# Kernel tuning notes

Hardware: AMD Instinct MI355X
Metric: run time of the kernel (lower is better)

## Reference

```python
import jax, jax.numpy as jnp
import numpy as np
from functools import partial

B, L, D = 4, 1024, 512
H = 8                 # attention heads
DIN = 2 * D           # mamba d_inner (expand=2)
N = 16                # mamba d_state
K = 4                 # mamba d_conv
R = 32                # dt_rank = ceil(D/16)


def setup_inputs() -> dict:
    key = jax.random.key(0)
    ks = jax.random.split(key, 24)
    s = 0.02
    nrm = lambda k, sh: (jax.random.normal(k, sh, dtype=jnp.float32) * s)
    inp = {
        'x':       jax.random.normal(ks[0], (B, L, D), dtype=jnp.float32),
        # attention projections
        'Wq': nrm(ks[1], (D, D)), 'bq': jnp.zeros((D,), jnp.float32),
        'Wk': nrm(ks[2], (D, D)), 'bk': jnp.zeros((D,), jnp.float32),
        'Wv': nrm(ks[3], (D, D)), 'bv': jnp.zeros((D,), jnp.float32),
        'Wo': nrm(ks[4], (D, D)), 'bo': jnp.zeros((D,), jnp.float32),
        # layernorms
        'ln1_g': jnp.ones((D,), jnp.float32), 'ln1_b': jnp.zeros((D,), jnp.float32),
        'ln2_g': jnp.ones((D,), jnp.float32), 'ln2_b': jnp.zeros((D,), jnp.float32),
        # mamba params
        'm_Win':   nrm(ks[5], (D, 2 * DIN)),            # in_proj (no bias)
        'm_conv_w': nrm(ks[6], (DIN, 1, K)),            # depthwise causal conv
        'm_conv_b': jnp.zeros((DIN,), jnp.float32),
        'm_Wx':    nrm(ks[7], (DIN, R + 2 * N)),        # x_proj (no bias)
        'm_Wdt':   nrm(ks[8], (R, DIN)),                # dt_proj
        'm_bdt':   jnp.full((DIN,), 0.5, jnp.float32),
        'm_Alog':  jnp.log(jnp.broadcast_to(jnp.arange(1, N + 1, dtype=jnp.float32), (DIN, N))).copy(),
        'm_D':     jnp.ones((DIN,), jnp.float32),
        'm_Wout':  nrm(ks[9], (DIN, D)),                # out_proj (no bias)
    }
    return inp


def _layernorm(x, g, b, eps=1e-5):
    mu = jnp.mean(x, axis=-1, keepdims=True)
    var = jnp.var(x, axis=-1, keepdims=True)
    return (x - mu) * jax.lax.rsqrt(var + eps) * g + b


def _mamba(x, Win, conv_w, conv_b, Wx, Wdt, bdt, Alog, Dp, Wout):
    b, l, _ = x.shape
    xz = x @ Win                           # [B,L,2*DIN]
    xi, z = xz[..., :DIN], xz[..., DIN:]
    # causal depthwise conv over time
    xt = jnp.transpose(xi, (0, 2, 1))      # [B,DIN,L]
    xt = jax.lax.conv_general_dilated(
        xt, conv_w, window_strides=(1,), padding=[(K - 1, 0)],
        feature_group_count=DIN, dimension_numbers=('NCH', 'OIH', 'NCH'))
    xc = jax.nn.silu(jnp.transpose(xt, (0, 2, 1)) + conv_b)   # [B,L,DIN]
    # input-dependent SSM params
    dbl = xc @ Wx                          # [B,L,R+2N]
    dt = jax.nn.softplus(dbl[..., :R] @ Wdt + bdt)            # [B,L,DIN]
    Bm = dbl[..., R:R + N]                 # [B,L,N]
    Cm = dbl[..., R + N:]                  # [B,L,N]
    A = -jnp.exp(Alog)                     # [DIN,N]
    dA = jnp.exp(dt[..., None] * A)                     # [B,L,DIN,N]
    dBx = (dt * xc)[..., None] * Bm[:, :, None, :]      # [B,L,DIN,N]

    def step(h, t):
        dA_t, dBx_t, C_t = t
        h = h * dA_t + dBx_t               # [B,DIN,N]
        y = jnp.einsum('bdn,bn->bd', h, C_t)
        return h, y

    h0 = jnp.zeros((b, DIN, N), xc.dtype)
    _, ys = jax.lax.scan(step, h0, (jnp.swapaxes(dA, 0, 1),
                                    jnp.swapaxes(dBx, 0, 1),
                                    jnp.swapaxes(Cm, 0, 1)))
    y = jnp.swapaxes(ys, 0, 1)             # [B,L,DIN]
    y = y + xc * Dp
    y = y * jax.nn.silu(z)
    return y @ Wout                        # [B,L,D]


def reference(x, Wq, bq, Wk, bk, Wv, bv, Wo, bo, ln1_g, ln1_b, ln2_g, ln2_b,
              m_Win, m_conv_w, m_conv_b, m_Wx, m_Wdt, m_bdt, m_Alog, m_D, m_Wout):
    b, l, d = x.shape
    E = d // H
    q = (x @ Wq + bq).reshape(b, l, H, E)
    k = (x @ Wk + bk).reshape(b, l, H, E)
    v = (x @ Wv + bv).reshape(b, l, H, E)
    scores = jnp.einsum('blhe,bshe->bhls', q, k) * (E ** -0.5)
    attn = jax.nn.softmax(scores, axis=-1)                    # [B,H,L,L]
    o = jnp.einsum('bhls,bshe->blhe', attn, v).reshape(b, l, d)
    new_x = o @ Wo + bo
    x1 = _layernorm(x + new_x, ln1_g, ln1_b)
    y = _mamba(x1, m_Win, m_conv_w, m_conv_b, m_Wx, m_Wdt, m_bdt, m_Alog, m_D, m_Wout)
    out = _layernorm(x1 + y, ln2_g, ln2_b)
    return out, attn
```

## Files before the change

kernel.cpp:

```cpp
#include <hip/hip_runtime.h>
#include <hip/hip_bf16.h>

#define BB 4
#define LL 1024
#define DD 512
#define HH 8
#define EE 64
#define DIN 1024
#define NN 16
#define KK 4
#define RR 32
#define BL (BB*LL)
#define CC 32
#define LC (LL/CC)
#define BDN (BB*DIN*NN)

using bf16 = __hip_bfloat16;
typedef __attribute__((ext_vector_type(8))) short short8;
typedef __attribute__((ext_vector_type(4))) float f32x4;

__device__ __forceinline__ float ldf(const float* p) { return *p; }
__device__ __forceinline__ float ldf(const bf16* p) { return __bfloat162float(*p); }
__device__ __forceinline__ void stf(float* p, float v) { *p = v; }
__device__ __forceinline__ void stf(bf16* p, float v) { *p = __float2bfloat16(v); }
__device__ __forceinline__ short f2bs(float f) { bf16 h = __float2bfloat16(f); return *(short*)&h; }

__global__ void cvt_k(const float* __restrict__ in, bf16* __restrict__ out, int n)
{
    int i = blockIdx.x * 256 + threadIdx.x;
    if (i < n) out[i] = __float2bfloat16(in[i]);
}

__global__ void tpw_k(const float* __restrict__ in, bf16* __restrict__ outT,
                      int Kd, int Nd)
{
    __shared__ float t[32][33];
    const int n0 = blockIdx.x * 32, k0 = blockIdx.y * 32;
    const int tx = threadIdx.x & 31, ty = threadIdx.x >> 5;
#pragma unroll
    for (int i = 0; i < 4; ++i)
        t[ty + 8 * i][tx] = in[(size_t)(k0 + ty + 8 * i) * Nd + n0 + tx];
    __syncthreads();
#pragma unroll
    for (int i = 0; i < 4; ++i)
        outT[(size_t)(n0 + ty + 8 * i) * Kd + k0 + tx] = __float2bfloat16(t[tx][ty + 8 * i]);
}

__global__ void tpv_k(const bf16* __restrict__ v, bf16* __restrict__ vT)
{
    __shared__ float t[32][33];
    const int l0 = blockIdx.x * 32;
    const int e0 = blockIdx.y * 32;
    const int bh = blockIdx.z, b = bh >> 3, h = bh & 7;
    const int tx = threadIdx.x & 31, ty = threadIdx.x >> 5;
#pragma unroll
    for (int i = 0; i < 4; ++i)
        t[ty + 8 * i][tx] = ldf(&v[(size_t)(b * LL + l0 + ty + 8 * i) * DD + h * EE + e0 + tx]);
    __syncthreads();
#pragma unroll
    for (int i = 0; i < 4; ++i)
        stf(&vT[(size_t)(bh * EE + e0 + ty + 8 * i) * LL + l0 + tx], t[tx][ty + 8 * i]);
}

template <typename TC>
__global__ void mfma_gemm_k(const bf16* __restrict__ A, int lda,
                            const bf16* __restrict__ Bt, int ldb,
                            const float* __restrict__ bias,
                            TC* __restrict__ C, int ldc, int Kd)
{
    const int lane = threadIdx.x & 63;
    const int w = threadIdx.x >> 6;
    const int m = lane & 15, quad = lane >> 4;
    const int m0 = blockIdx.y * 64 + (w >> 1) * 32;
    const int n0 = blockIdx.x * 64 + (w & 1) * 32;
    f32x4 acc[2][2] = {};
    const bf16* a0p = A + (size_t)(m0 + m) * lda + quad * 8;
    const bf16* a1p = a0p + (size_t)16 * lda;
    const bf16* b0p = Bt + (size_t)(n0 + m) * ldb + quad * 8;
    const bf16* b1p = b0p + (size_t)16 * ldb;
    for (int k = 0; k < Kd; k += 32) {
        short8 a0 = *(const short8*)(a0p + k);
        short8 a1 = *(const short8*)(a1p + k);
        short8 b0 = *(const short8*)(b0p + k);
        short8 b1 = *(const short8*)(b1p + k);
        acc[0][0] = __builtin_amdgcn_mfma_f32_16x16x32_bf16(a0, b0, acc[0][0], 0, 0, 0);
        acc[0][1] = __builtin_amdgcn_mfma_f32_16x16x32_bf16(a0, b1, acc[0][1], 0, 0, 0);
        acc[1][0] = __builtin_amdgcn_mfma_f32_16x16x32_bf16(a1, b0, acc[1][0], 0, 0, 0);
        acc[1][1] = __builtin_amdgcn_mfma_f32_16x16x32_bf16(a1, b1, acc[1][1], 0, 0, 0);
    }
#pragma unroll
    for (int i = 0; i < 2; ++i)
#pragma unroll
        for (int j = 0; j < 2; ++j)
#pragma unroll
            for (int r = 0; r < 4; ++r) {
                int row = m0 + i * 16 + quad * 4 + r;
                int col = n0 + j * 16 + (lane & 15);
                float vv = acc[i][j][r] + (bias ? bias[col] : 0.f);
                stf(&C[(size_t)row * ldc + col], vv);
            }
}

__global__ void attn_fused_k(const bf16* __restrict__ q, const bf16* __restrict__ k,
                             const bf16* __restrict__ vT,
                             float* __restrict__ attn, bf16* __restrict__ o)
{
    const int rt = blockIdx.x;
    const int bh = blockIdx.y, b = bh >> 3, h = bh & 7;
    const int w = threadIdx.x >> 6;
    const int lane = threadIdx.x & 63;
    const int m = lane & 15, quad = lane >> 4;
    __shared__ float pm[4][16], ps[4][16];
    __shared__ bf16 P[16][1032];

    const bf16* qp = q + (size_t)(b * LL + rt * 16 + m) * DD + h * EE + quad * 8;
    short8 a0 = *(const short8*)(qp);
    short8 a1 = *(const short8*)(qp + 32);

    f32x4 acc[16];
#pragma unroll
    for (int t = 0; t < 16; ++t) {
        int srow = w * 256 + t * 16 + m;
        const bf16* kp = k + (size_t)(b * LL + srow) * DD + h * EE + quad * 8;
        short8 b0 = *(const short8*)(kp);
        short8 b1 = *(const short8*)(kp + 32);
        f32x4 c = {};
        c = __builtin_amdgcn_mfma_f32_16x16x32_bf16(a0, b0, c, 0, 0, 0);
        c = __builtin_amdgcn_mfma_f32_16x16x32_bf16(a1, b1, c, 0, 0, 0);
        acc[t] = c;
    }

#pragma unroll
    for (int r = 0; r < 4; ++r) {
        float mx = -1e30f;
#pragma unroll
        for (int t = 0; t < 16; ++t) { acc[t][r] *= 0.125f; mx = fmaxf(mx, acc[t][r]); }
        mx = fmaxf(mx, __shfl_xor(mx, 1)); mx = fmaxf(mx, __shfl_xor(mx, 2));
        mx = fmaxf(mx, __shfl_xor(mx, 4)); mx = fmaxf(mx, __shfl_xor(mx, 8));
        if (m == 0) pm[w][quad * 4 + r] = mx;
    }
    __syncthreads();
#pragma unroll
    for (int r = 0; r < 4; ++r) {
        float mx = fmaxf(fmaxf(pm[0][quad * 4 + r], pm[1][quad * 4 + r]),
                         fmaxf(pm[2][quad * 4 + r], pm[3][quad * 4 + r]));
        float s = 0.f;
#pragma unroll
        for (int t = 0; t < 16; ++t) { float e = __expf(acc[t][r] - mx); acc[t][r] = e; s += e; }
        s += __shfl_xor(s, 1); s += __shfl_xor(s, 2);
        s += __shfl_xor(s, 4); s += __shfl_xor(s, 8);
        if (m == 0) ps[w][quad * 4 + r] = s;
    }
    __syncthreads();
#pragma unroll
    for (int r = 0; r < 4; ++r) {
        float tot = ps[0][quad * 4 + r] + ps[1][quad * 4 + r] + ps[2][quad * 4 + r] + ps[3][quad * 4 + r];
        float inv = 1.f / tot;
        int row = rt * 16 + quad * 4 + r;
        float* op = attn + ((size_t)bh * LL + row) * LL + w * 256 + (lane & 15);
#pragma unroll
        for (int t = 0; t < 16; ++t) {
            float pv = acc[t][r] * inv;
            op[t * 16] = pv;
            P[quad * 4 + r][w * 256 + t * 16 + m] = __float2bfloat16(pv);
        }
    }
    __syncthreads();

    const bf16* vp = vT + (size_t)(bh * EE + w * 16 + m) * LL + quad * 8;
    f32x4 oacc = {};
    for (int k0 = 0; k0 < LL; k0 += 32) {
        short8 af = *(const short8*)(&P[m][k0 + quad * 8]);
        short8 bf = *(const short8*)(vp + k0);
        oacc = __builtin_amdgcn_mfma_f32_16x16x32_bf16(af, bf, oacc, 0, 0, 0);
    }
#pragma unroll
    for (int r = 0; r < 4; ++r) {
        int row = rt * 16 + quad * 4 + r;
        stf(&o[(size_t)(b * LL + row) * DD + h * EE + w * 16 + (lane & 15)], oacc[r]);
    }
}

template <typename TA, typename TC, bool SP>
__global__ void gemm_k(const TA* __restrict__ A, int lda,
                       const float* __restrict__ B, int ldb,
                       const float* __restrict__ bias,
                       TC* __restrict__ C, int ldc,
                       int M, int N, int Kd)
{
    __shared__ float As[32][33];
    __shared__ float Bs[32][33];
    const int tid = threadIdx.x;
    const int tx = tid & 31;
    const int ty = tid >> 5;
    const int rowBase = blockIdx.y * 32;
    const int colBase = blockIdx.x * 32;
    float acc[4] = {0.f, 0.f, 0.f, 0.f};

    for (int k0 = 0; k0 < Kd; k0 += 32) {
#pragma unroll
        for (int i = 0; i < 4; ++i) {
            int r = ty + 8 * i;
            As[r][tx] = ldf(&A[(size_t)(rowBase + r) * lda + k0 + tx]);
            Bs[r][tx] = B[(size_t)(k0 + r) * ldb + colBase + tx];
        }
        __syncthreads();
#pragma unroll 8
        for (int kk = 0; kk < 32; ++kk) {
            float bv = Bs[kk][tx];
#pragma unroll
            for (int i = 0; i < 4; ++i) acc[i] += As[ty + 8 * i][kk] * bv;
        }
        __syncthreads();
    }
#pragma unroll
    for (int i = 0; i < 4; ++i) {
        int row = rowBase + ty + 8 * i;
        int col = colBase + tx;
        float r = acc[i] + (bias ? bias[col] : 0.f);
        if (SP) r = (r > 20.f) ? r : log1pf(__expf(r));
        stf(&C[(size_t)row * ldc + col], r);
    }
}

template <typename TA, typename TR, typename TO>
__global__ void add_ln_k(const TA* __restrict__ a, const TR* __restrict__ r,
                         const float* __restrict__ g, const float* __restrict__ be,
                         TO* __restrict__ out)
{
    const int row = blockIdx.x;
    const int tid = threadIdx.x;
    __shared__ float red[256];
    const size_t base = (size_t)row * DD;
    float v0 = ldf(&a[base + tid]) + ldf(&r[base + tid]);
    float v1 = ldf(&a[base + 256 + tid]) + ldf(&r[base + 256 + tid]);
    red[tid] = v0 + v1;
    __syncthreads();
    for (int off = 128; off > 0; off >>= 1) {
        if (tid < off) red[tid] += red[tid + off];
        __syncthreads();
    }
    const float mu = red[0] * (1.f / 512.f);
    __syncthreads();
    float d0 = v0 - mu, d1 = v1 - mu;
    red[tid] = d0 * d0 + d1 * d1;
    __syncthreads();
    for (int off = 128; off > 0; off >>= 1) {
        if (tid < off) red[tid] += red[tid + off];
        __syncthreads();
    }
    const float rs = rsqrtf(red[0] * (1.f / 512.f) + 1e-5f);
    stf(&out[base + tid], d0 * rs * g[tid] + be[tid]);
    stf(&out[base + 256 + tid], d1 * rs * g[tid + 256] + be[tid + 256]);
}

__global__ void conv_silu_k(const bf16* __restrict__ xz,
                            const float* __restrict__ w,
                            const float* __restrict__ cb,
                            bf16* __restrict__ xc)
{
    const int idx = blockIdx.x * 256 + threadIdx.x;
    const int c = idx & (DIN - 1);
    const int t = (idx >> 10) & (LL - 1);
    const int b = idx >> 20;
    float acc = cb[c];
    const bf16* xi = xz + (size_t)b * LL * (2 * DIN) + c;
#pragma unroll
    for (int j = 0; j < KK; ++j) {
        int tt = t - (KK - 1) + j;
        if (tt >= 0) acc += w[c * KK + j] * ldf(&xi[(size_t)tt * (2 * DIN)]);
    }
    stf(&xc[idx], acc / (1.f + __expf(-acc)));
}

__global__ void scan_p1_k(const bf16* __restrict__ dt, const bf16* __restrict__ xc,
                          const float* __restrict__ dbl, const float* __restrict__ Alog,
                          float* __restrict__ P, float* __restrict__ S)
{
    const int d = (blockIdx.x & 3) * 256 + threadIdx.x;
    const int c = blockIdx.x >> 2;
    const int b = blockIdx.y;
    float A[NN];
#pragma unroll
    for (int n = 0; n < NN; ++n) A[n] = -__expf(Alog[d * NN + n]);
    const int t0 = c * LC;
    const bf16* dt_b = dt + ((size_t)b * LL + t0) * DIN + d;
    const bf16* xc_b = xc + ((size_t)b * LL + t0) * DIN + d;
    const float* dbl_b = dbl + ((size_t)b * LL + t0) * 64 + RR;
    float h[NN];
#pragma unroll
    for (int n = 0; n < NN; ++n) h[n] = 0.f;
    float sdt = 0.f;
#pragma unroll 4
    for (int t = 0; t < LC; ++t) {
        float dtv = ldf(&dt_b[(size_t)t * DIN]);
        float xcv = ldf(&xc_b[(size_t)t * DIN]);
        float dtx = dtv * xcv;
        sdt += dtv;
#pragma unroll
        for (int n = 0; n < NN; ++n) {
            float dA = __expf(dtv * A[n]);
            h[n] = h[n] * dA + dtx * dbl_b[(size_t)t * 64 + n];
        }
    }
    float* Pp = P + (size_t)c * BDN + ((size_t)(b * DIN + d)) * NN;
    float* Sp = S + (size_t)c * BDN + ((size_t)(b * DIN + d)) * NN;
#pragma unroll
    for (int n = 0; n < NN; ++n) { Pp[n] = __expf(sdt * A[n]); Sp[n] = h[n]; }
}

__global__ void scan_p2_k(const float* __restrict__ P, const float* __restrict__ S,
                          float* __restrict__ Hc)
{
    const size_t bdn = (size_t)blockIdx.x * 256 + threadIdx.x;
    float h = 0.f;
#pragma unroll
    for (int c = 0; c < CC; ++c) {
        Hc[(size_t)c * BDN + bdn] = h;
        h = S[(size_t)c * BDN + bdn] + P[(size_t)c * BDN + bdn] * h;
    }
}

__global__ void scan_p3_k(const bf16* __restrict__ dt, const bf16* __restrict__ xc,
                          const float* __restrict__ dbl, const float* __restrict__ Alog,
                          const float* __restrict__ Dv, const float* __restrict__ Hc,
                          bf16* __restrict__ xzm)
{
    const int d = (blockIdx.x & 3) * 256 + threadIdx.x;
    const int c = blockIdx.x >> 2;
    const int b = blockIdx.y;
    float A[NN];
#pragma unroll
    for (int n = 0; n < NN; ++n) A[n] = -__expf(Alog[d * NN + n]);
    const float Dp = Dv[d];
    const int t0 = c * LC;
    const bf16* dt_b = dt + ((size_t)b * LL + t0) * DIN + d;
    const bf16* xc_b = xc + ((size_t)b * LL + t0) * DIN + d;
    const float* dbl_b = dbl + ((size_t)b * LL + t0) * 64 + RR;
    bf16* xz_b = xzm + ((size_t)b * LL + t0) * (2 * DIN);
    const float* hp = Hc + (size_t)c * BDN + ((size_t)(b * DIN + d)) * NN;
    float h[NN];
#pragma unroll
    for (int n = 0; n < NN; ++n) h[n] = hp[n];
#pragma unroll 2
    for (int t = 0; t < LC; ++t) {
        float dtv = ldf(&dt_b[(size_t)t * DIN]);
        float xcv = ldf(&xc_b[(size_t)t * DIN]);
        float dtx = dtv * xcv;
        float y = 0.f;
#pragma unroll
        for (int n = 0; n < NN; ++n) {
            float dA = __expf(dtv * A[n]);
            h[n] = h[n] * dA + dtx * dbl_b[(size_t)t * 64 + n];
            y += h[n] * dbl_b[(size_t)t * 64 + NN + n];
        }
        float zv = ldf(&xz_b[(size_t)t * (2 * DIN) + DIN + d]);
        float yv = y + xcv * Dp;
        yv *= zv / (1.f + __expf(-zv));
        stf(&xz_b[(size_t)t * (2 * DIN) + d], yv);
    }
}

extern "C" void kernel_launch(void* const* d_in, const int* in_sizes, int n_in,
                              void* d_out, int out_size, void* d_ws, size_t ws_size,
                              hipStream_t stream)
{
    const float* x    = (const float*)d_in[0];
    const float* Wq   = (const float*)d_in[1];
    const float* bq   = (const float*)d_in[2];
    const float* Wk   = (const float*)d_in[3];
    const float* bk   = (const float*)d_in[4];
    const float* Wv   = (const float*)d_in[5];
    const float* bv   = (const float*)d_in[6];
    const float* Wo   = (const float*)d_in[7];
    const float* bo   = (const float*)d_in[8];
    const float* g1   = (const float*)d_in[9];
    const float* b1   = (const float*)d_in[10];
    const float* g2   = (const float*)d_in[11];
    const float* b2   = (const float*)d_in[12];
    const float* Win  = (const float*)d_in[13];
    const float* cw   = (const float*)d_in[14];
    const float* cb   = (const float*)d_in[15];
    const float* Wx   = (const float*)d_in[16];
    const float* Wdt  = (const float*)d_in[17];
    const float* bdt  = (const float*)d_in[18];
    const float* Alog = (const float*)d_in[19];
    const float* Dv   = (const float*)d_in[20];
    const float* Wout = (const float*)d_in[21];

    float* out  = (float*)d_out;
    float* attn = out + (size_t)BL * DD;

    const size_t M1 = 1048576;
    bf16* wsb = (bf16*)d_ws;
    bf16* xb   = wsb;
    bf16* q    = wsb + 2*M1;
    bf16* kb   = wsb + 4*M1;
    bf16* v    = wsb + 6*M1;
    bf16* o    = wsb + 8*M1;
    bf16* x1   = wsb + 10*M1;
    bf16* xz   = wsb + 12*M1;
    bf16* xc   = wsb + 20*M1;
    bf16* dtb  = wsb + 24*M1;
    float* dbl = (float*)(wsb + 28*M1);
    bf16* vT   = wsb + 28*M1 + 524288;
    bf16* Wqt  = vT + 2*M1;
    bf16* Wkt  = Wqt + 262144;
    bf16* Wvt  = Wkt + 262144;
    bf16* Wot  = Wvt + 262144;
    bf16* Wint = Wot + 262144;
    bf16* Wxt  = Wint + M1;
    bf16* Woutt= Wxt + 65536;
    bf16* newx = q;
    bf16* ym   = v;
    float* Pp = (float*)xb;
    float* Sp = (float*)kb;
    float* Hc = (float*)vT;

    const dim3 blk(256);

    cvt_k<<<dim3(BL*DD/256), blk, 0, stream>>>(x, xb, BL*DD);
    tpw_k<<<dim3(DD/32, DD/32),  blk, 0, stream>>>(Wq,   Wqt,  DD, DD);
    tpw_k<<<dim3(DD/32, DD/32),  blk, 0, stream>>>(Wk,   Wkt,  DD, DD);
    tpw_k<<<dim3(DD/32, DD/32),  blk, 0, stream>>>(Wv,   Wvt,  DD, DD);
    tpw_k<<<dim3(DD/32, DD/32),  blk, 0, stream>>>(Wo,   Wot,  DD, DD);
    tpw_k<<<dim3(2*DIN/32, DD/32), blk, 0, stream>>>(Win, Wint, DD, 2*DIN);
    tpw_k<<<dim3(64/32, DIN/32), blk, 0, stream>>>(Wx,   Wxt,  DIN, 64);
    tpw_k<<<dim3(DD/32, DIN/32), blk, 0, stream>>>(Wout, Woutt, DIN, DD);

    mfma_gemm_k<bf16><<<dim3(DD/64, BL/64), blk, 0, stream>>>(xb, DD, Wqt, DD, bq, q,  DD, DD);
    mfma_gemm_k<bf16><<<dim3(DD/64, BL/64), blk, 0, stream>>>(xb, DD, Wkt, DD, bk, kb, DD, DD);
    mfma_gemm_k<bf16><<<dim3(DD/64, BL/64), blk, 0, stream>>>(xb, DD, Wvt, DD, bv, v,  DD, DD);
    tpv_k<<<dim3(LL/32, EE/32, BB*HH), blk, 0, stream>>>(v, vT);

    attn_fused_k<<<dim3(LL/16, BB*HH), blk, 0, stream>>>(q, kb, vT, attn, o);

    mfma_gemm_k<bf16><<<dim3(DD/64, BL/64), blk, 0, stream>>>(o, DD, Wot, DD, bo, newx, DD, DD);
    add_ln_k<float, bf16, bf16><<<dim3(BL), blk, 0, stream>>>(x, newx, g1, b1, x1);

    mfma_gemm_k<bf16><<<dim3(2*DIN/64, BL/64), blk, 0, stream>>>(x1, DD, Wint, DD, nullptr, xz, 2*DIN, DD);

    conv_silu_k<<<dim3(BL*DIN/256), blk, 0, stream>>>(xz, cw, cb, xc);

    mfma_gemm_k<float><<<dim3(64/64, BL/64), blk, 0, stream>>>(xc, DIN, Wxt, DIN, nullptr, dbl, 64, DIN);

    gemm_k<float, bf16, true><<<dim3(DIN/32, BL/32), blk, 0, stream>>>(dbl, 64, Wdt, DIN, bdt, dtb, DIN, BL, DIN, RR);

    scan_p1_k<<<dim3((DIN/256)*CC, BB), blk, 0, stream>>>(dtb, xc, dbl, Alog, Pp, Sp);
    scan_p2_k<<<dim3(BDN/256), blk, 0, stream>>>(Pp, Sp, Hc);
    scan_p3_k<<<dim3((DIN/256)*CC, BB), blk, 0, stream>>>(dtb, xc, dbl, Alog, Dv, Hc, xz);

    mfma_gemm_k<bf16><<<dim3(DD/64, BL/64), blk, 0, stream>>>(xz, 2*DIN, Woutt, DIN, nullptr, ym, DD, DIN);

    add_ln_k<bf16, bf16, float><<<dim3(BL), blk, 0, stream>>>(x1, ym, g2, b2, out);
}
```

Baseline: 564.9 us.

## Use 128x128 MFMA GEMM tiles, batch QKV projections and weight transposes

Adds a 128x128-tile MFMA GEMM in which each wave computes a 64x64 subtile (4x4 accumulators), raising operand reuse per load. The Q/K/V projections run as a single launch over grid z, relying on Wqt/Wkt/Wvt being contiguous and on q/kb/v sitting at a fixed 2*M1 stride apart. The seven weight-transpose launches are merged into one job-table kernel. The aim is fewer launches and less global-load traffic per FLOP, at the cost of more register pressure and fewer blocks for the smaller GEMMs, which could hurt occupancy.

```diff
diff --git a/kernel.cpp b/kernel.cpp
--- a/kernel.cpp
+++ b/kernel.cpp
@@ -23,7 +23,6 @@
 __device__ __forceinline__ float ldf(const bf16* p) { return __bfloat162float(*p); }
 __device__ __forceinline__ void stf(float* p, float v) { *p = v; }
 __device__ __forceinline__ void stf(bf16* p, float v) { *p = __float2bfloat16(v); }
-__device__ __forceinline__ short f2bs(float f) { bf16 h = __float2bfloat16(f); return *(short*)&h; }
 
 __global__ void cvt_k(const float* __restrict__ in, bf16* __restrict__ out, int n)
 {
@@ -31,19 +30,29 @@
     if (i < n) out[i] = __float2bfloat16(in[i]);
 }
 
-__global__ void tpw_k(const float* __restrict__ in, bf16* __restrict__ outT,
-                      int Kd, int Nd)
-{
+struct TpwJob { const float* in; bf16* out; int Kd, Nd, gx, tile0; };
+struct TpwJobs { TpwJob j[7]; };
+
+__global__ void tpw_batch_k(TpwJobs jobs)
+{
+    const int tile = blockIdx.x;
+    int ji = 0;
+#pragma unroll
+    for (int i = 1; i < 7; ++i) if (tile >= jobs.j[i].tile0) ji = i;
+    const TpwJob jb = jobs.j[ji];
+    const int lt = tile - jb.tile0;
+    const int n0 = (lt % jb.gx) * 32;
+    const int k0 = (lt / jb.gx) * 32;
+
     __shared__ float t[32][33];
-    const int n0 = blockIdx.x * 32, k0 = blockIdx.y * 32;
     const int tx = threadIdx.x & 31, ty = threadIdx.x >> 5;
 #pragma unroll
     for (int i = 0; i < 4; ++i)
-        t[ty + 8 * i][tx] = in[(size_t)(k0 + ty + 8 * i) * Nd + n0 + tx];
+        t[ty + 8 * i][tx] = jb.in[(size_t)(k0 + ty + 8 * i) * jb.Nd + n0 + tx];
     __syncthreads();
 #pragma unroll
     for (int i = 0; i < 4; ++i)
-        outT[(size_t)(n0 + ty + 8 * i) * Kd + k0 + tx] = __float2bfloat16(t[tx][ty + 8 * i]);
+        jb.out[(size_t)(n0 + ty + 8 * i) * jb.Kd + k0 + tx] = __float2bfloat16(t[tx][ty + 8 * i]);
 }
 
 __global__ void tpv_k(const bf16* __restrict__ v, bf16* __restrict__ vT)
@@ -60,6 +69,57 @@
 #pragma unroll
     for (int i = 0; i < 4; ++i)
         stf(&vT[(size_t)(bh * EE + e0 + ty + 8 * i) * LL + l0 + tx], t[tx][ty + 8 * i]);
+}
+
+template <typename TC>
+__global__ void mfma_gemm128_k(const bf16* __restrict__ A, int lda,
+                               const bf16* __restrict__ Bt0, size_t bstride, int ldb,
+                               const float* __restrict__ bias0,
+                               const float* __restrict__ bias1,
+                               const float* __restrict__ bias2,
+                               TC* __restrict__ C0, size_t cstride, int ldc, int Kd)
+{
+    const int z = blockIdx.z;
+    const bf16* Bt = Bt0 + (size_t)z * bstride;
+    TC* C = C0 + (size_t)z * cstride;
+    const float* bias = (z == 0) ? bias0 : (z == 1) ? bias1 : bias2;
+
+    const int lane = threadIdx.x & 63;
+    const int w = threadIdx.x >> 6;
+    const int m = lane & 15, quad = lane >> 4;
+    const int m0 = blockIdx.y * 128 + (w >> 1) * 64;
+    const int n0 = blockIdx.x * 128 + (w & 1) * 64;
+
+    f32x4 acc[4][4] = {};
+    const bf16* ap = A + (size_t)(m0 + m) * lda + quad * 8;
+    const bf16* bp = Bt + (size_t)(n0 + m) * ldb + quad * 8;
+    const size_t rsa = (size_t)16 * lda;
+    const size_t rsb = (size_t)16 * ldb;
+    for (int k = 0; k < Kd; k += 32) {
+        short8 a[4], b[4];
+#pragma unroll
+        for (int i = 0; i < 4; ++i) a[i] = *(const short8*)(ap + i * rsa + k);
+#pragma unroll
+        for (int j = 0; j < 4; ++j) b[j] = *(const short8*)(bp + j * rsb + k);
+#pragma unroll
+        for (int i = 0; i < 4; ++i)
+#pragma unroll
+            for (int j = 0; j < 4; ++j)
+                acc[i][j] = __builtin_amdgcn_mfma_f32_16x16x32_bf16(a[i], b[j], acc[i][j], 0, 0, 0);
+    }
+    float bv[4];
+#pragma unroll
+    for (int j = 0; j < 4; ++j) bv[j] = bias ? bias[n0 + j * 16 + m] : 0.f;
+#pragma unroll
+    for (int i = 0; i < 4; ++i)
+#pragma unroll
+        for (int j = 0; j < 4; ++j)
+#pragma unroll
+            for (int r = 0; r < 4; ++r) {
+                int row = m0 + i * 16 + quad * 4 + r;
+                int col = n0 + j * 16 + m;
+                stf(&C[(size_t)row * ldc + col], acc[i][j][r] + bv[j]);
+            }
 }
 
 template <typename TC>
@@ -420,25 +480,34 @@
     const dim3 blk(256);
 
     cvt_k<<<dim3(BL*DD/256), blk, 0, stream>>>(x, xb, BL*DD);
-    tpw_k<<<dim3(DD/32, DD/32),  blk, 0, stream>>>(Wq,   Wqt,  DD, DD);
-    tpw_k<<<dim3(DD/32, DD/32),  blk, 0, stream>>>(Wk,   Wkt,  DD, DD);
-    tpw_k<<<dim3(DD/32, DD/32),  blk, 0, stream>>>(Wv,   Wvt,  DD, DD);
-    tpw_k<<<dim3(DD/32, DD/32),  blk, 0, stream>>>(Wo,   Wot,  DD, DD);
-    tpw_k<<<dim3(2*DIN/32, DD/32), blk, 0, stream>>>(Win, Wint, DD, 2*DIN);
-    tpw_k<<<dim3(64/32, DIN/32), blk, 0, stream>>>(Wx,   Wxt,  DIN, 64);
-    tpw_k<<<dim3(DD/32, DIN/32), blk, 0, stream>>>(Wout, Woutt, DIN, DD);
-
-    mfma_gemm_k<bf16><<<dim3(DD/64, BL/64), blk, 0, stream>>>(xb, DD, Wqt, DD, bq, q,  DD, DD);
-    mfma_gemm_k<bf16><<<dim3(DD/64, BL/64), blk, 0, stream>>>(xb, DD, Wkt, DD, bk, kb, DD, DD);
-    mfma_gemm_k<bf16><<<dim3(DD/64, BL/64), blk, 0, stream>>>(xb, DD, Wvt, DD, bv, v,  DD, DD);
+    TpwJobs tj;
+    int t0 = 0, nj = 0;
+    auto addjob = [&](const float* in, bf16* outp, int Kd, int Nd) {
+        tj.j[nj] = {in, outp, Kd, Nd, Nd / 32, t0};
+        t0 += (Nd / 32) * (Kd / 32);
+        ++nj;
+    };
+    addjob(Wq,   Wqt,   DD,  DD);
+    addjob(Wk,   Wkt,   DD,  DD);
+    addjob(Wv,   Wvt,   DD,  DD);
+    addjob(Wo,   Wot,   DD,  DD);
+    addjob(Win,  Wint,  DD,  2*DIN);
+    addjob(Wx,   Wxt,   DIN, 64);
+    addjob(Wout, Woutt, DIN, DD);
+    tpw_batch_k<<<dim3(t0), blk, 0, stream>>>(tj);
+
+    mfma_gemm128_k<bf16><<<dim3(DD/128, BL/128, 3), blk, 0, stream>>>(
+        xb, DD, Wqt, (size_t)DD*DD, DD, bq, bk, bv, q, (size_t)2*M1, DD, DD);
     tpv_k<<<dim3(LL/32, EE/32, BB*HH), blk, 0, stream>>>(v, vT);
 
     attn_fused_k<<<dim3(LL/16, BB*HH), blk, 0, stream>>>(q, kb, vT, attn, o);
 
-    mfma_gemm_k<bf16><<<dim3(DD/64, BL/64), blk, 0, stream>>>(o, DD, Wot, DD, bo, newx, DD, DD);
+    mfma_gemm128_k<bf16><<<dim3(DD/128, BL/128, 1), blk, 0, stream>>>(
+        o, DD, Wot, 0, DD, bo, nullptr, nullptr, newx, 0, DD, DD);
     add_ln_k<float, bf16, bf16><<<dim3(BL), blk, 0, stream>>>(x, newx, g1, b1, x1);
 
-    mfma_gemm_k<bf16><<<dim3(2*DIN/64, BL/64), blk, 0, stream>>>(x1, DD, Wint, DD, nullptr, xz, 2*DIN, DD);
+    mfma_gemm128_k<bf16><<<dim3(2*DIN/128, BL/128, 1), blk, 0, stream>>>(
+        x1, DD, Wint, 0, DD, nullptr, nullptr, nullptr, xz, 0, 2*DIN, DD);
 
     conv_silu_k<<<dim3(BL*DIN/256), blk, 0, stream>>>(xz, cw, cb, xc);
 
@@ -450,7 +519,8 @@
     scan_p2_k<<<dim3(BDN/256), blk, 0, stream>>>(Pp, Sp, Hc);
     scan_p3_k<<<dim3((DIN/256)*CC, BB), blk, 0, stream>>>(dtb, xc, dbl, Alog, Dv, Hc, xz);
 
-    mfma_gemm_k<bf16><<<dim3(DD/64, BL/64), blk, 0, stream>>>(xz, 2*DIN, Woutt, DIN, nullptr, ym, DD, DIN);
+    mfma_gemm128_k<bf16><<<dim3(DD/128, BL/128, 1), blk, 0, stream>>>(
+        xz, 2*DIN, Woutt, 0, DIN, nullptr, nullptr, nullptr, ym, 0, DD, DIN);
 
     add_ln_k<bf16, bf16, float><<<dim3(BL), blk, 0, stream>>>(x1, ym, g2, b2, out);
 }
```

After: 517.5 us. 8.4% less time.
